# Kernel optimization log

Measured on AMD Instinct MI355X. Metric: run time of the kernel, lower is better.

Reference implementation:

```python
import jax, jax.numpy as jnp
import numpy as np

N_NODES = 50000
N_EDGES = 625000
F_IN = 128
HID = 128
N_GRAPHS = 128
N_CLASSES = 10


def _init_linear(key, fan_in, fan_out, bias=True):
    k1, k2 = jax.random.split(key)
    lim = 1.0 / np.sqrt(fan_in)
    W = jax.random.uniform(k1, (fan_in, fan_out), jnp.float32, -lim, lim)
    if bias:
        b = jax.random.uniform(k2, (fan_out,), jnp.float32, -lim, lim)
        return W, b
    return W


def setup_inputs() -> dict:
    key = jax.random.key(0)
    ks = jax.random.split(key, 12)
    x = jax.random.normal(ks[0], (N_NODES, F_IN), jnp.float32)
    edge_index = jax.random.randint(ks[1], (2, N_EDGES), 0, N_NODES, jnp.int64)
    batch = jnp.sort(jax.random.randint(ks[2], (N_NODES,), 0, N_GRAPHS, jnp.int64))
    # GraphConv k: lin_rel (weight+bias) applied to aggregated neighbors, lin_root (no bias) applied to x
    W1r, b1 = _init_linear(ks[3], F_IN, HID)
    W1s = _init_linear(ks[4], F_IN, HID, bias=False)
    W2r, b2 = _init_linear(ks[5], HID, HID)
    W2s = _init_linear(ks[6], HID, HID, bias=False)
    W3r, b3 = _init_linear(ks[7], HID, HID)
    W3s = _init_linear(ks[8], HID, HID, bias=False)
    L1w, L1b = _init_linear(ks[9], 2 * HID, 128)
    L2w, L2b = _init_linear(ks[10], 128, 64)
    L3w, L3b = _init_linear(ks[11], 64, N_CLASSES)
    return {"x": x, "edge_index": edge_index, "batch": batch,
            "W1r": W1r, "b1": b1, "W1s": W1s,
            "W2r": W2r, "b2": b2, "W2s": W2s,
            "W3r": W3r, "b3": b3, "W3s": W3s,
            "L1w": L1w, "L1b": L1b, "L2w": L2w, "L2b": L2b,
            "L3w": L3w, "L3b": L3b}


def _graph_conv(x, src, dst, Wr, br, Ws):
    # sum-aggregate source node features at destination nodes, then transform
    agg = jax.ops.segment_sum(x[src], dst, num_segments=N_NODES)  # [N, F]
    return agg @ Wr + br + x @ Ws


def _pool(x, batch):
    # cat([global_max_pool, global_mean_pool])
    mx = jax.ops.segment_max(x, batch, num_segments=N_GRAPHS)
    mx = jnp.where(jnp.isfinite(mx), mx, 0.0)  # guard empty segments
    sm = jax.ops.segment_sum(x, batch, num_segments=N_GRAPHS)
    cnt = jax.ops.segment_sum(jnp.ones((x.shape[0],), x.dtype), batch,
                              num_segments=N_GRAPHS)
    mean = sm / jnp.maximum(cnt, 1.0)[:, None]
    return jnp.concatenate([mx, mean], axis=1)  # [G, 2F]


def reference(x, edge_index, batch, W1r, b1, W1s, W2r, b2, W2s, W3r, b3, W3s,
              L1w, L1b, L2w, L2b, L3w, L3b):
    src, dst = edge_index[0], edge_index[1]
    h = jax.nn.relu(_graph_conv(x, src, dst, W1r, b1, W1s))
    x1 = _pool(h, batch)
    h = jax.nn.relu(_graph_conv(h, src, dst, W2r, b2, W2s))
    x2 = _pool(h, batch)
    h = jax.nn.relu(_graph_conv(h, src, dst, W3r, b3, W3s))
    x3 = _pool(h, batch)
    g = x1 + x2 + x3                      # [G, 256]
    g = jax.nn.relu(g @ L1w + L1b)        # dropout is identity at inference
    g = jax.nn.relu(g @ L2w + L2b)
    return jax.nn.log_softmax(g @ L3w + L3b, axis=-1)
```

## Files before the change

kernel.cpp:

```cpp
#include <hip/hip_runtime.h>
#include <math.h>

constexpr int N  = 50000;
constexpr int NE = 625000;
constexpr int F  = 128;
constexpr int NG = 128;
constexpr int NC = 10;
constexpr int CAP = 48;

typedef __attribute__((ext_vector_type(4))) float f32x4;
typedef __attribute__((ext_vector_type(8))) short bf16x8;

__device__ __forceinline__ ushort f2bf(float f) {
    unsigned u = __float_as_uint(f);
    u = (u + 0x7FFF + ((u >> 16) & 1)) >> 16;
    return (ushort)u;
}
__device__ __forceinline__ float bf_lo(unsigned u) {
    return __uint_as_float(u << 16);
}
__device__ __forceinline__ float bf_hi(unsigned u) {
    return __uint_as_float(u & 0xffff0000u);
}


__global__ __launch_bounds__(256) void k_setup(
    const float* __restrict__ x, ushort* __restrict__ xb,
    const float* __restrict__ W0, const float* __restrict__ W1,
    const float* __restrict__ W2, const float* __restrict__ W3,
    const float* __restrict__ W4, const float* __restrict__ W5,
    ushort* __restrict__ O,
    const int* __restrict__ batch, int* __restrict__ gstart,
    int* __restrict__ cnt, float* __restrict__ gpool,
    int* __restrict__ csrb, ushort* __restrict__ hA, ushort* __restrict__ hB)
{
    int b = blockIdx.x, t = threadIdx.x;
    if (b < 3125) {
        int i = (b * 256 + t) * 8;
        float4 a = *(const float4*)(x + i);
        float4 c = *(const float4*)(x + i + 4);
        ushort r[8] = {f2bf(a.x), f2bf(a.y), f2bf(a.z), f2bf(a.w),
                       f2bf(c.x), f2bf(c.y), f2bf(c.z), f2bf(c.w)};
        *(uint4*)(xb + i) = *(uint4*)r;
    } else if (b < 3509) {
        int bb = b - 3125;
        int wsel = bb >> 6;
        int i = (bb & 63) * 256 + t;
        int k = i >> 7, n = i & 127;
        const float* W = wsel == 0 ? W0 : wsel == 1 ? W1 : wsel == 2 ? W2
                       : wsel == 3 ? W3 : wsel == 4 ? W4 : W5;
        O[wsel * 16384 + n * 128 + k] = f2bf(W[k * 128 + n]);
    } else if (b == 3509) {
        int g = t;
        if (g > NG) return;
        if (g == NG) { gstart[NG] = N; return; }
        int lo = 0, hi = N;
        while (lo < hi) {
            int mid = (lo + hi) >> 1;
            if (batch[mid] < g) lo = mid + 1; else hi = mid;
        }
        gstart[g] = lo;
    } else if (b < 3706) {
        int i = (b - 3510) * 256 + t;
        if (i < N) cnt[i] = 0;
    } else if (b < 3770) {
        int i = (b - 3706) * 256 + t;
        *(uint4*)((unsigned*)gpool + i * 4) = (uint4){0, 0, 0, 0};
    } else if (b < 6114) {
        int i = (b - 3770) * 256 + t;
        if (i < N * CAP / 4)
            *(int4*)(csrb + i * 4) = (int4){N, N, N, N};
    } else {
        if (t < 48) {
            int which = t >> 4, j = t & 15;
            ushort* tab = which == 0 ? xb : which == 1 ? hA : hB;
            *(uint4*)(tab + (size_t)N * F + j * 8) = (uint4){0, 0, 0, 0};
        }
    }
}


__global__ void k_fill(const int* __restrict__ src, const int* __restrict__ dst,
                       int* __restrict__ cnt, int* __restrict__ csrb, int ne) {
    int e = blockIdx.x * blockDim.x + threadIdx.x;
    if (e < ne) {
        int d = dst[e];
        int pos = atomicAdd(&cnt[d], 1);
        if (pos < CAP) csrb[d * CAP + pos] = src[e];
    }
}


#define LDSTR 136

__global__ __launch_bounds__(256) void k_layer(
    const ushort* __restrict__ hin,
    const int* __restrict__ cnt, const int* __restrict__ csrb,
    const int* __restrict__ batch, const int* __restrict__ gstart,
    const ushort* __restrict__ WrT, const ushort* __restrict__ WsT,
    const float* __restrict__ br,
    ushort* __restrict__ hout,
    float* __restrict__ gmaxL,
    float* __restrict__ gsum,
    int nrows)
{
    __shared__ ushort sA[16][LDSTR];
    __shared__ int sbatch[16];

    const int tid = threadIdx.x;
    const int r0 = blockIdx.x * 16;
    const int wv = tid >> 6, lane = tid & 63;
    const int lo16 = lane & 15, hi = lane >> 4;

    if (tid < 16) {
        int r = r0 + tid;
        sbatch[tid] = (r < nrows) ? batch[r] : -1;
    }

    {
        int row = wv * 4 + hi;
        int v = r0 + row;
        float acc[8] = {0.f, 0.f, 0.f, 0.f, 0.f, 0.f, 0.f, 0.f};
        if (v < nrows) {
            int deg = cnt[v];
            if (deg > CAP) deg = CAP;
            const int* bucket = csrb + v * CAP;
            for (int e = 0; e < deg; e += 16) {
                int4 i0 = *(const int4*)(bucket + e);
                int4 i1 = *(const int4*)(bucket + e + 4);
                int4 i2 = *(const int4*)(bucket + e + 8);
                int4 i3 = *(const int4*)(bucket + e + 12);
                int idx[16] = {i0.x, i0.y, i0.z, i0.w, i1.x, i1.y, i1.z, i1.w,
                               i2.x, i2.y, i2.z, i2.w, i3.x, i3.y, i3.z, i3.w};
                uint4 w[16];
#pragma unroll
                for (int j = 0; j < 16; ++j)
                    w[j] = *(const uint4*)(hin + (size_t)idx[j] * F + lo16 * 8);
#pragma unroll
                for (int j = 0; j < 16; ++j) {
                    acc[0] += bf_lo(w[j].x); acc[1] += bf_hi(w[j].x);
                    acc[2] += bf_lo(w[j].y); acc[3] += bf_hi(w[j].y);
                    acc[4] += bf_lo(w[j].z); acc[5] += bf_hi(w[j].z);
                    acc[6] += bf_lo(w[j].w); acc[7] += bf_hi(w[j].w);
                }
            }
        }
        ushort r8[8];
#pragma unroll
        for (int j = 0; j < 8; ++j) r8[j] = f2bf(acc[j]);
        *(uint4*)(&sA[row][lo16 * 8]) = *(uint4*)r8;
    }

    bf16x8 af1[4];
    {
        int row = r0 + lo16;
#pragma unroll
        for (int ks = 0; ks < 4; ++ks) {
            if (row < nrows)
                af1[ks] = *(const bf16x8*)(hin + (size_t)row * F + ks * 32 + hi * 8);
            else
                af1[ks] = (bf16x8){0, 0, 0, 0, 0, 0, 0, 0};
        }
    }

    f32x4 acc2[2];
#pragma unroll
    for (int n = 0; n < 2; ++n) {
        float b = br[wv * 32 + n * 16 + lo16];
        acc2[n] = (f32x4){b, b, b, b};
    }

    __syncthreads();

#pragma unroll
    for (int ks = 0; ks < 4; ++ks) {
        int k0 = ks * 32 + hi * 8;
        bf16x8 a0 = *(const bf16x8*)(&sA[lo16][k0]);
#pragma unroll
        for (int n = 0; n < 2; ++n) {
            bf16x8 b = *(const bf16x8*)(WrT + (size_t)(wv * 32 + n * 16 + lo16) * F + k0);
            acc2[n] = __builtin_amdgcn_mfma_f32_16x16x32_bf16(a0, b, acc2[n], 0, 0, 0);
        }
    }

#pragma unroll
    for (int ks = 0; ks < 4; ++ks) {
        int k0 = ks * 32 + hi * 8;
#pragma unroll
        for (int n = 0; n < 2; ++n) {
            bf16x8 b = *(const bf16x8*)(WsT + (size_t)(wv * 32 + n * 16 + lo16) * F + k0);
            acc2[n] = __builtin_amdgcn_mfma_f32_16x16x32_bf16(af1[ks], b, acc2[n], 0, 0, 0);
        }
    }

    __syncthreads();

#pragma unroll
    for (int n = 0; n < 2; ++n) {
        int col = wv * 32 + n * 16 + lo16;
#pragma unroll
        for (int q = 0; q < 4; ++q) {
            int lrow = hi * 4 + q;
            sA[lrow][col] = f2bf(fmaxf(acc2[n][q], 0.f));
        }
    }
    __syncthreads();

    if (hout) {
        int row = tid >> 4;
        int c = (tid & 15) * 8;
        int grow = r0 + row;
        if (grow < nrows)
            *(uint4*)(hout + (size_t)grow * F + c) = *(const uint4*)(&sA[row][c]);
    }

    {
        int f = tid & 127, seg = tid >> 7;
        int curg = -1;
        float mx = 0.f, sm = 0.f;
        for (int r = seg * 8; r < seg * 8 + 8; ++r) {
            int bg = sbatch[r];
            if (bg != curg) {
                if (curg >= 0) {
                    float inv = 1.0f / (float)(gstart[curg + 1] - gstart[curg]);
                    atomicMax((int*)&gmaxL[curg * 128 + f], __float_as_int(mx));
                    atomicAdd(&gsum[curg * 128 + f], sm * inv);
                }
                curg = bg; mx = 0.f; sm = 0.f;
            }
            if (bg >= 0) {
                float v = bf_lo((unsigned)sA[r][f]);
                mx = fmaxf(mx, v);
                sm += v;
            }
        }
        if (curg >= 0) {
            float inv = 1.0f / (float)(gstart[curg + 1] - gstart[curg]);
            atomicMax((int*)&gmaxL[curg * 128 + f], __float_as_int(mx));
            atomicAdd(&gsum[curg * 128 + f], sm * inv);
        }
    }
}


__global__ __launch_bounds__(256) void k_mlp(const float* __restrict__ gpool,
                                             const float* __restrict__ L1w, const float* __restrict__ L1b,
                                             const float* __restrict__ L2w, const float* __restrict__ L2b,
                                             const float* __restrict__ L3w, const float* __restrict__ L3b,
                                             float* __restrict__ out) {
    __shared__ float gv[256], o1[128], o2[64], o3[16];
    int g = blockIdx.x, t = threadIdx.x;
    if (t < 128) {
        gv[t] = gpool[16384 + g * 128 + t] + gpool[2 * 16384 + g * 128 + t]
              + gpool[3 * 16384 + g * 128 + t];
    } else {
        gv[t] = gpool[g * 128 + (t - 128)];
    }
    __syncthreads();
    if (t < 128) {
        float a = L1b[t];
        for (int k = 0; k < 256; ++k) a += gv[k] * L1w[k * 128 + t];
        o1[t] = fmaxf(a, 0.f);
    }
    __syncthreads();
    if (t < 64) {
        float a = L2b[t];
        for (int k = 0; k < 128; ++k) a += o1[k] * L2w[k * 64 + t];
        o2[t] = fmaxf(a, 0.f);
    }
    __syncthreads();
    if (t < NC) {
        float a = L3b[t];
        for (int k = 0; k < 64; ++k) a += o2[k] * L3w[k * NC + t];
        o3[t] = a;
    }
    __syncthreads();
    if (t < NC) {
        float m = o3[0];
        for (int i = 1; i < NC; ++i) m = fmaxf(m, o3[i]);
        float s = 0.f;
        for (int i = 0; i < NC; ++i) s += expf(o3[i] - m);
        out[g * NC + t] = o3[t] - m - logf(s);
    }
}


extern "C" void kernel_launch(void* const* d_in, const int* in_sizes, int n_in,
                              void* d_out, int out_size, void* d_ws, size_t ws_size,
                              hipStream_t stream) {
    const float* x     = (const float*)d_in[0];
    const int*   ei    = (const int*)d_in[1];
    const int*   batch = (const int*)d_in[2];
    const float* W1r = (const float*)d_in[3];
    const float* b1  = (const float*)d_in[4];
    const float* W1s = (const float*)d_in[5];
    const float* W2r = (const float*)d_in[6];
    const float* b2  = (const float*)d_in[7];
    const float* W2s = (const float*)d_in[8];
    const float* W3r = (const float*)d_in[9];
    const float* b3  = (const float*)d_in[10];
    const float* W3s = (const float*)d_in[11];
    const float* L1w = (const float*)d_in[12];
    const float* L1b = (const float*)d_in[13];
    const float* L2w = (const float*)d_in[14];
    const float* L2b = (const float*)d_in[15];
    const float* L3w = (const float*)d_in[16];
    const float* L3b = (const float*)d_in[17];
    float* out = (float*)d_out;

    char* ws = (char*)d_ws;
    const size_t SZ_HB = (size_t)(N + 8) * F * sizeof(ushort);
    ushort* x_bf  = (ushort*)(ws);
    ushort* hA    = (ushort*)(ws + SZ_HB);
    ushort* hB    = (ushort*)(ws + 2 * SZ_HB);
    size_t off    = 3 * SZ_HB;
    ushort* Wt0   = (ushort*)(ws + off); off += 6 * 128 * 128 * 2;
    int* cnt      = (int*)(ws + off); off += 200704;
    int* csrb     = (int*)(ws + off); off += (size_t)N * CAP * 4;
    int* gstart   = (int*)(ws + off); off += 1024;
    float* gpool  = (float*)(ws + off); off += 4 * 16384 * 4;

    const int* src = ei;
    const int* dst = ei + NE;

    k_setup<<<6115, 256, 0, stream>>>(x, x_bf, W1r, W1s, W2r, W2s, W3r, W3s, Wt0,
                                      batch, gstart, cnt, gpool, csrb, hA, hB);

    k_fill<<<(NE + 255) / 256, 256, 0, stream>>>(src, dst, cnt, csrb, NE);

    const int NLB = (N + 15) / 16;
    ushort* Wt[6];
    for (int i = 0; i < 6; ++i) Wt[i] = Wt0 + i * 16384;

    k_layer<<<NLB, 256, 0, stream>>>(x_bf, cnt, csrb, batch, gstart,
                                     Wt[0], Wt[1], b1, hA,
                                     gpool + 16384, gpool, N);
    k_layer<<<NLB, 256, 0, stream>>>(hA, cnt, csrb, batch, gstart,
                                     Wt[2], Wt[3], b2, hB,
                                     gpool + 2 * 16384, gpool, N);
    k_layer<<<NLB, 256, 0, stream>>>(hB, cnt, csrb, batch, gstart,
                                     Wt[4], Wt[5], b3, (ushort*)nullptr,
                                     gpool + 3 * 16384, gpool, N);

    k_mlp<<<NG, 256, 0, stream>>>(gpool, L1w, L1b, L2w, L2b, L3w, L3b, out);
}
```

Measured before the change: 204.6 us.

## Split layer into column-blocked gather and conv-pool kernels with 16-bit edge indices

Node feature tables are stored column-blocked (four 32-feature slabs of 64 bytes per node), so each gather pass touches a smaller slab that fits cache better. Neighbor aggregation moves into a separate k_gather kernel that reduces across lanes with shuffles and writes an aggregate buffer. A k_convpool kernel then runs the MFMA transform and pooling. Bucket indices shrink to ushort, which relies on N fitting in 16 bits. The cost is an extra aggregate write and read per layer plus three more kernel launches.

```diff
diff --git a/kernel.cpp b/kernel.cpp
--- a/kernel.cpp
+++ b/kernel.cpp
@@ -1,26 +1,35 @@
 #include <hip/hip_runtime.h>
 #include <math.h>
 
-constexpr int N  = 50000;
-constexpr int NE = 625000;
-constexpr int F  = 128;
-constexpr int NG = 128;
-constexpr int NC = 10;
+constexpr int N   = 50000;
+constexpr int NP1 = N + 1;
+constexpr int NE  = 625000;
+constexpr int F   = 128;
+constexpr int NG  = 128;
+constexpr int NC  = 10;
 constexpr int CAP = 48;
 
 typedef __attribute__((ext_vector_type(4))) float f32x4;
 typedef __attribute__((ext_vector_type(8))) short bf16x8;
+typedef __attribute__((ext_vector_type(4))) unsigned u32x4;
 
 __device__ __forceinline__ ushort f2bf(float f) {
     unsigned u = __float_as_uint(f);
     u = (u + 0x7FFF + ((u >> 16) & 1)) >> 16;
     return (ushort)u;
 }
-__device__ __forceinline__ float bf_lo(unsigned u) {
-    return __uint_as_float(u << 16);
-}
-__device__ __forceinline__ float bf_hi(unsigned u) {
-    return __uint_as_float(u & 0xffff0000u);
+__device__ __forceinline__ float bf_lo(unsigned u) { return __uint_as_float(u << 16); }
+__device__ __forceinline__ float bf_hi(unsigned u) { return __uint_as_float(u & 0xffff0000u); }
+
+__device__ __forceinline__ size_t tIdx(int cb, int node, int off) {
+    return ((size_t)cb * NP1 + node) * 32 + off;
+}
+
+__device__ __forceinline__ void accum8(float* acc, uint4 w) {
+    acc[0] += bf_lo(w.x); acc[1] += bf_hi(w.x);
+    acc[2] += bf_lo(w.y); acc[3] += bf_hi(w.y);
+    acc[4] += bf_lo(w.z); acc[5] += bf_hi(w.z);
+    acc[6] += bf_lo(w.w); acc[7] += bf_hi(w.w);
 }
 
 
@@ -32,16 +41,19 @@
     ushort* __restrict__ O,
     const int* __restrict__ batch, int* __restrict__ gstart,
     int* __restrict__ cnt, float* __restrict__ gpool,
-    int* __restrict__ csrb, ushort* __restrict__ hA, ushort* __restrict__ hB)
+    ushort* __restrict__ bkt, ushort* __restrict__ hA, ushort* __restrict__ hB)
 {
     int b = blockIdx.x, t = threadIdx.x;
     if (b < 3125) {
-        int i = (b * 256 + t) * 8;
-        float4 a = *(const float4*)(x + i);
-        float4 c = *(const float4*)(x + i + 4);
+        int i = b * 256 + t;
+        int node = i >> 4, col8 = i & 15;
+        int c0 = col8 * 8;
+        const float* xp = x + (size_t)node * F + c0;
+        float4 a = *(const float4*)(xp);
+        float4 c = *(const float4*)(xp + 4);
         ushort r[8] = {f2bf(a.x), f2bf(a.y), f2bf(a.z), f2bf(a.w),
                        f2bf(c.x), f2bf(c.y), f2bf(c.z), f2bf(c.w)};
-        *(uint4*)(xb + i) = *(uint4*)r;
+        *(uint4*)(xb + tIdx(c0 >> 5, node, c0 & 31)) = *(uint4*)r;
     } else if (b < 3509) {
         int bb = b - 3125;
         int wsel = bb >> 6;
@@ -66,43 +78,93 @@
     } else if (b < 3770) {
         int i = (b - 3706) * 256 + t;
         *(uint4*)((unsigned*)gpool + i * 4) = (uint4){0, 0, 0, 0};
-    } else if (b < 6114) {
+    } else if (b < 4942) {
         int i = (b - 3770) * 256 + t;
-        if (i < N * CAP / 4)
-            *(int4*)(csrb + i * 4) = (int4){N, N, N, N};
+        if (i < N * CAP / 8) {
+            unsigned p = 0xC350C350u;
+            *(uint4*)(bkt + (size_t)i * 8) = (uint4){p, p, p, p};
+        }
     } else {
         if (t < 48) {
-            int which = t >> 4, j = t & 15;
-            ushort* tab = which == 0 ? xb : which == 1 ? hA : hB;
-            *(uint4*)(tab + (size_t)N * F + j * 8) = (uint4){0, 0, 0, 0};
+            int table = t >> 4, r = t & 15;
+            int cb = r >> 2, j = r & 3;
+            ushort* tab = table == 0 ? xb : table == 1 ? hA : hB;
+            *(uint4*)(tab + tIdx(cb, N, j * 8)) = (uint4){0, 0, 0, 0};
         }
     }
 }
 
 
 __global__ void k_fill(const int* __restrict__ src, const int* __restrict__ dst,
-                       int* __restrict__ cnt, int* __restrict__ csrb, int ne) {
+                       int* __restrict__ cnt, ushort* __restrict__ bkt, int ne) {
     int e = blockIdx.x * blockDim.x + threadIdx.x;
     if (e < ne) {
         int d = dst[e];
         int pos = atomicAdd(&cnt[d], 1);
-        if (pos < CAP) csrb[d * CAP + pos] = src[e];
+        if (pos < CAP) bkt[(size_t)d * CAP + pos] = (ushort)src[e];
+    }
+}
+
+
+__global__ __launch_bounds__(256) void k_gather(
+    const ushort* __restrict__ tab, const int* __restrict__ cnt,
+    const ushort* __restrict__ bkt, ushort* __restrict__ aggB)
+{
+    const int b = blockIdx.x;
+    const int cb = b / 6250;
+    const int nb = b - cb * 6250;
+    const int tid = threadIdx.x;
+    const int lane = tid & 63, wv = tid >> 6;
+    const int g  = lane >> 5;
+    const int e8 = (lane >> 2) & 7;
+    const int j  = lane & 3;
+
+    const int v = nb * 8 + wv * 2 + g;
+    const int deg = min(cnt[v], CAP);
+    const ushort* bucket = bkt + (size_t)v * CAP;
+    const ushort* tcb = tab + (size_t)cb * NP1 * 32;
+
+    float acc[8] = {0.f, 0.f, 0.f, 0.f, 0.f, 0.f, 0.f, 0.f};
+
+    int i0 = __builtin_nontemporal_load(bucket + e8);
+    int i1 = __builtin_nontemporal_load(bucket + 8 + e8);
+    uint4 w0 = *(const uint4*)(tcb + (size_t)i0 * 32 + j * 8);
+    uint4 w1 = *(const uint4*)(tcb + (size_t)i1 * 32 + j * 8);
+    accum8(acc, w0);
+    accum8(acc, w1);
+
+    for (int e = 16; e < deg; e += 8) {
+        int ii = __builtin_nontemporal_load(bucket + e + e8);
+        uint4 w = *(const uint4*)(tcb + (size_t)ii * 32 + j * 8);
+        accum8(acc, w);
+    }
+
+#pragma unroll
+    for (int k = 0; k < 8; ++k) {
+        acc[k] += __shfl_xor(acc[k], 4, 64);
+        acc[k] += __shfl_xor(acc[k], 8, 64);
+        acc[k] += __shfl_xor(acc[k], 16, 64);
+    }
+
+    if ((lane & 28) == 0) {
+        ushort r8[8];
+#pragma unroll
+        for (int k = 0; k < 8; ++k) r8[k] = f2bf(acc[k]);
+        u32x4 val = *(u32x4*)r8;
+        __builtin_nontemporal_store(val, (u32x4*)(aggB + tIdx(cb, v, j * 8)));
     }
 }
 
 
 #define LDSTR 136
 
-__global__ __launch_bounds__(256) void k_layer(
-    const ushort* __restrict__ hin,
-    const int* __restrict__ cnt, const int* __restrict__ csrb,
+__global__ __launch_bounds__(256) void k_convpool(
+    const ushort* __restrict__ aggB, const ushort* __restrict__ hinB,
     const int* __restrict__ batch, const int* __restrict__ gstart,
     const ushort* __restrict__ WrT, const ushort* __restrict__ WsT,
     const float* __restrict__ br,
-    ushort* __restrict__ hout,
-    float* __restrict__ gmaxL,
-    float* __restrict__ gsum,
-    int nrows)
+    ushort* __restrict__ houtB,
+    float* __restrict__ gmaxL, float* __restrict__ gsum)
 {
     __shared__ ushort sA[16][LDSTR];
     __shared__ int sbatch[16];
@@ -112,55 +174,14 @@
     const int wv = tid >> 6, lane = tid & 63;
     const int lo16 = lane & 15, hi = lane >> 4;
 
-    if (tid < 16) {
-        int r = r0 + tid;
-        sbatch[tid] = (r < nrows) ? batch[r] : -1;
-    }
-
-    {
-        int row = wv * 4 + hi;
-        int v = r0 + row;
-        float acc[8] = {0.f, 0.f, 0.f, 0.f, 0.f, 0.f, 0.f, 0.f};
-        if (v < nrows) {
-            int deg = cnt[v];
-            if (deg > CAP) deg = CAP;
-            const int* bucket = csrb + v * CAP;
-            for (int e = 0; e < deg; e += 16) {
-                int4 i0 = *(const int4*)(bucket + e);
-                int4 i1 = *(const int4*)(bucket + e + 4);
-                int4 i2 = *(const int4*)(bucket + e + 8);
-                int4 i3 = *(const int4*)(bucket + e + 12);
-                int idx[16] = {i0.x, i0.y, i0.z, i0.w, i1.x, i1.y, i1.z, i1.w,
-                               i2.x, i2.y, i2.z, i2.w, i3.x, i3.y, i3.z, i3.w};
-                uint4 w[16];
-#pragma unroll
-                for (int j = 0; j < 16; ++j)
-                    w[j] = *(const uint4*)(hin + (size_t)idx[j] * F + lo16 * 8);
-#pragma unroll
-                for (int j = 0; j < 16; ++j) {
-                    acc[0] += bf_lo(w[j].x); acc[1] += bf_hi(w[j].x);
-                    acc[2] += bf_lo(w[j].y); acc[3] += bf_hi(w[j].y);
-                    acc[4] += bf_lo(w[j].z); acc[5] += bf_hi(w[j].z);
-                    acc[6] += bf_lo(w[j].w); acc[7] += bf_hi(w[j].w);
-                }
-            }
-        }
-        ushort r8[8];
-#pragma unroll
-        for (int j = 0; j < 8; ++j) r8[j] = f2bf(acc[j]);
-        *(uint4*)(&sA[row][lo16 * 8]) = *(uint4*)r8;
-    }
-
-    bf16x8 af1[4];
-    {
-        int row = r0 + lo16;
-#pragma unroll
-        for (int ks = 0; ks < 4; ++ks) {
-            if (row < nrows)
-                af1[ks] = *(const bf16x8*)(hin + (size_t)row * F + ks * 32 + hi * 8);
-            else
-                af1[ks] = (bf16x8){0, 0, 0, 0, 0, 0, 0, 0};
-        }
+    if (tid < 16) sbatch[tid] = batch[r0 + tid];
+
+    const int rowa = r0 + lo16;
+    bf16x8 af0[4], af1[4];
+#pragma unroll
+    for (int ks = 0; ks < 4; ++ks) {
+        af0[ks] = *(const bf16x8*)(aggB + tIdx(ks, rowa, hi * 8));
+        af1[ks] = *(const bf16x8*)(hinB + tIdx(ks, rowa, hi * 8));
     }
 
     f32x4 acc2[2];
@@ -170,49 +191,39 @@
         acc2[n] = (f32x4){b, b, b, b};
     }
 
-    __syncthreads();
-
 #pragma unroll
     for (int ks = 0; ks < 4; ++ks) {
         int k0 = ks * 32 + hi * 8;
-        bf16x8 a0 = *(const bf16x8*)(&sA[lo16][k0]);
 #pragma unroll
         for (int n = 0; n < 2; ++n) {
-            bf16x8 b = *(const bf16x8*)(WrT + (size_t)(wv * 32 + n * 16 + lo16) * F + k0);
-            acc2[n] = __builtin_amdgcn_mfma_f32_16x16x32_bf16(a0, b, acc2[n], 0, 0, 0);
-        }
-    }
-
+            bf16x8 bR = *(const bf16x8*)(WrT + (size_t)(wv * 32 + n * 16 + lo16) * F + k0);
+            acc2[n] = __builtin_amdgcn_mfma_f32_16x16x32_bf16(af0[ks], bR, acc2[n], 0, 0, 0);
+        }
+    }
 #pragma unroll
     for (int ks = 0; ks < 4; ++ks) {
         int k0 = ks * 32 + hi * 8;
 #pragma unroll
         for (int n = 0; n < 2; ++n) {
-            bf16x8 b = *(const bf16x8*)(WsT + (size_t)(wv * 32 + n * 16 + lo16) * F + k0);
-            acc2[n] = __builtin_amdgcn_mfma_f32_16x16x32_bf16(af1[ks], b, acc2[n], 0, 0, 0);
-        }
-    }
-
-    __syncthreads();
+            bf16x8 bS = *(const bf16x8*)(WsT + (size_t)(wv * 32 + n * 16 + lo16) * F + k0);
+            acc2[n] = __builtin_amdgcn_mfma_f32_16x16x32_bf16(af1[ks], bS, acc2[n], 0, 0, 0);
+        }
+    }
 
 #pragma unroll
     for (int n = 0; n < 2; ++n) {
         int col = wv * 32 + n * 16 + lo16;
 #pragma unroll
-        for (int q = 0; q < 4; ++q) {
-            int lrow = hi * 4 + q;
-            sA[lrow][col] = f2bf(fmaxf(acc2[n][q], 0.f));
-        }
-    }
-    __syncthreads();
-
-    if (hout) {
-        int row = tid >> 4;
-        int c = (tid & 15) * 8;
-        int grow = r0 + row;
-        if (grow < nrows)
-            *(uint4*)(hout + (size_t)grow * F + c) = *(const uint4*)(&sA[row][c]);
-    }
+        for (int q = 0; q < 4; ++q)
+            sA[hi * 4 + q][col] = f2bf(fmaxf(acc2[n][q], 0.f));
+    }
+
+    if (houtB) {
+        int ns = lane >> 2, jj = lane & 3;
+        uint4 val = *(const uint4*)(&sA[ns][wv * 32 + jj * 8]);
+        *(uint4*)(houtB + tIdx(wv, r0 + ns, jj * 8)) = val;
+    }
+    __syncthreads();
 
     {
         int f = tid & 127, seg = tid >> 7;
@@ -228,11 +239,9 @@
                 }
                 curg = bg; mx = 0.f; sm = 0.f;
             }
-            if (bg >= 0) {
-                float v = bf_lo((unsigned)sA[r][f]);
-                mx = fmaxf(mx, v);
-                sm += v;
-            }
+            float v = bf_lo((unsigned)sA[r][f]);
+            mx = fmaxf(mx, v);
+            sm += v;
         }
         if (curg >= 0) {
             float inv = 1.0f / (float)(gstart[curg + 1] - gstart[curg]);
@@ -309,38 +318,39 @@
     float* out = (float*)d_out;
 
     char* ws = (char*)d_ws;
-    const size_t SZ_HB = (size_t)(N + 8) * F * sizeof(ushort);
+    const size_t SZ_TAB = (size_t)4 * NP1 * 32 * sizeof(ushort);
     ushort* x_bf  = (ushort*)(ws);
-    ushort* hA    = (ushort*)(ws + SZ_HB);
-    ushort* hB    = (ushort*)(ws + 2 * SZ_HB);
-    size_t off    = 3 * SZ_HB;
+    ushort* hA    = (ushort*)(ws + SZ_TAB);
+    ushort* hB    = (ushort*)(ws + 2 * SZ_TAB);
+    ushort* agg   = (ushort*)(ws + 3 * SZ_TAB);
+    size_t off    = 4 * SZ_TAB;
     ushort* Wt0   = (ushort*)(ws + off); off += 6 * 128 * 128 * 2;
     int* cnt      = (int*)(ws + off); off += 200704;
-    int* csrb     = (int*)(ws + off); off += (size_t)N * CAP * 4;
+    ushort* bkt   = (ushort*)(ws + off); off += (size_t)N * CAP * 2 + 256;
     int* gstart   = (int*)(ws + off); off += 1024;
     float* gpool  = (float*)(ws + off); off += 4 * 16384 * 4;
 
     const int* src = ei;
     const int* dst = ei + NE;
 
-    k_setup<<<6115, 256, 0, stream>>>(x, x_bf, W1r, W1s, W2r, W2s, W3r, W3s, Wt0,
-                                      batch, gstart, cnt, gpool, csrb, hA, hB);
-
-    k_fill<<<(NE + 255) / 256, 256, 0, stream>>>(src, dst, cnt, csrb, NE);
-
-    const int NLB = (N + 15) / 16;
+    k_setup<<<4943, 256, 0, stream>>>(x, x_bf, W1r, W1s, W2r, W2s, W3r, W3s, Wt0,
+                                      batch, gstart, cnt, gpool, bkt, hA, hB);
+    k_fill<<<(NE + 255) / 256, 256, 0, stream>>>(src, dst, cnt, bkt, NE);
+
     ushort* Wt[6];
     for (int i = 0; i < 6; ++i) Wt[i] = Wt0 + i * 16384;
-
-    k_layer<<<NLB, 256, 0, stream>>>(x_bf, cnt, csrb, batch, gstart,
-                                     Wt[0], Wt[1], b1, hA,
-                                     gpool + 16384, gpool, N);
-    k_layer<<<NLB, 256, 0, stream>>>(hA, cnt, csrb, batch, gstart,
-                                     Wt[2], Wt[3], b2, hB,
-                                     gpool + 2 * 16384, gpool, N);
-    k_layer<<<NLB, 256, 0, stream>>>(hB, cnt, csrb, batch, gstart,
-                                     Wt[4], Wt[5], b3, (ushort*)nullptr,
-                                     gpool + 3 * 16384, gpool, N);
+    const int NGB = 4 * 6250;
+    const int NCB = N / 16;
+
+    k_gather<<<NGB, 256, 0, stream>>>(x_bf, cnt, bkt, agg);
+    k_convpool<<<NCB, 256, 0, stream>>>(agg, x_bf, batch, gstart, Wt[0], Wt[1], b1,
+                                        hA, gpool + 16384, gpool);
+    k_gather<<<NGB, 256, 0, stream>>>(hA, cnt, bkt, agg);
+    k_convpool<<<NCB, 256, 0, stream>>>(agg, hA, batch, gstart, Wt[2], Wt[3], b2,
+                                        hB, gpool + 2 * 16384, gpool);
+    k_gather<<<NGB, 256, 0, stream>>>(hB, cnt, bkt, agg);
+    k_convpool<<<NCB, 256, 0, stream>>>(agg, hB, batch, gstart, Wt[4], Wt[5], b3,
+                                        (ushort*)nullptr, gpool + 3 * 16384, gpool);
 
     k_mlp<<<NG, 256, 0, stream>>>(gpool, L1w, L1b, L2w, L2b, L3w, L3b, out);
 }
```

New measurement: 264.1 us. +29.1%, slower.

## Store neighbor buckets as 16-bit indices and fuse edge fill into prep kernel

Applied to the files above, without the earlier changes.

Neighbor bucket indices are stored as 16-bit values instead of 32-bit, halving bucket memory for init, fill and the three layer gathers. The edge bucket fill is merged into the setup kernel, and a small separate init kernel now does the count and bucket clearing. Node indices up to 50000 fit in 16 bits, with 50000 (0xC350) used as the padding sentinel. This adds an extra launch and ties the code to a node count below 65536.

```diff
diff --git a/kernel.cpp b/kernel.cpp
--- a/kernel.cpp
+++ b/kernel.cpp
@@ -1,11 +1,11 @@
 #include <hip/hip_runtime.h>
 #include <math.h>
 
-constexpr int N  = 50000;
-constexpr int NE = 625000;
-constexpr int F  = 128;
-constexpr int NG = 128;
-constexpr int NC = 10;
+constexpr int N   = 50000;
+constexpr int NE  = 625000;
+constexpr int F   = 128;
+constexpr int NG  = 128;
+constexpr int NC  = 10;
 constexpr int CAP = 48;
 
 typedef __attribute__((ext_vector_type(4))) float f32x4;
@@ -16,41 +16,67 @@
     u = (u + 0x7FFF + ((u >> 16) & 1)) >> 16;
     return (ushort)u;
 }
-__device__ __forceinline__ float bf_lo(unsigned u) {
-    return __uint_as_float(u << 16);
-}
-__device__ __forceinline__ float bf_hi(unsigned u) {
-    return __uint_as_float(u & 0xffff0000u);
-}
-
-
-__global__ __launch_bounds__(256) void k_setup(
+__device__ __forceinline__ float bf_lo(unsigned u) { return __uint_as_float(u << 16); }
+__device__ __forceinline__ float bf_hi(unsigned u) { return __uint_as_float(u & 0xffff0000u); }
+
+__device__ __forceinline__ void accum8(float* acc, uint4 w) {
+    acc[0] += bf_lo(w.x); acc[1] += bf_hi(w.x);
+    acc[2] += bf_lo(w.y); acc[3] += bf_hi(w.y);
+    acc[4] += bf_lo(w.z); acc[5] += bf_hi(w.z);
+    acc[6] += bf_lo(w.w); acc[7] += bf_hi(w.w);
+}
+
+
+__global__ __launch_bounds__(256) void k_init(int* __restrict__ cnt,
+                                              ushort* __restrict__ bkt) {
+    int i = blockIdx.x * 256 + threadIdx.x;
+    const int NBKT = N * CAP / 8;
+    if (i < NBKT) {
+        unsigned p = 0xC350C350u;
+        *(uint4*)(bkt + (size_t)i * 8) = (uint4){p, p, p, p};
+    } else if (i < NBKT + 12512) {
+        int c = i - NBKT;
+        if (c * 4 < N + 4) *(uint4*)((unsigned*)cnt + c * 4) = (uint4){0, 0, 0, 0};
+    }
+}
+
+
+__global__ __launch_bounds__(256) void k_prep(
+    const int* __restrict__ src, const int* __restrict__ dst,
+    int* __restrict__ cnt, ushort* __restrict__ bkt,
     const float* __restrict__ x, ushort* __restrict__ xb,
     const float* __restrict__ W0, const float* __restrict__ W1,
     const float* __restrict__ W2, const float* __restrict__ W3,
     const float* __restrict__ W4, const float* __restrict__ W5,
     ushort* __restrict__ O,
     const int* __restrict__ batch, int* __restrict__ gstart,
-    int* __restrict__ cnt, float* __restrict__ gpool,
-    int* __restrict__ csrb, ushort* __restrict__ hA, ushort* __restrict__ hB)
+    float* __restrict__ gpool,
+    ushort* __restrict__ hA, ushort* __restrict__ hB)
 {
     int b = blockIdx.x, t = threadIdx.x;
-    if (b < 3125) {
-        int i = (b * 256 + t) * 8;
+    if (b < 2442) {
+        int e = b * 256 + t;
+        if (e < NE) {
+            int d = dst[e];
+            int pos = atomicAdd(&cnt[d], 1);
+            if (pos < CAP) bkt[(size_t)d * CAP + pos] = (ushort)src[e];
+        }
+    } else if (b < 5567) {
+        int i = ((b - 2442) * 256 + t) * 8;
         float4 a = *(const float4*)(x + i);
         float4 c = *(const float4*)(x + i + 4);
         ushort r[8] = {f2bf(a.x), f2bf(a.y), f2bf(a.z), f2bf(a.w),
                        f2bf(c.x), f2bf(c.y), f2bf(c.z), f2bf(c.w)};
         *(uint4*)(xb + i) = *(uint4*)r;
-    } else if (b < 3509) {
-        int bb = b - 3125;
+    } else if (b < 5951) {
+        int bb = b - 5567;
         int wsel = bb >> 6;
         int i = (bb & 63) * 256 + t;
         int k = i >> 7, n = i & 127;
         const float* W = wsel == 0 ? W0 : wsel == 1 ? W1 : wsel == 2 ? W2
                        : wsel == 3 ? W3 : wsel == 4 ? W4 : W5;
         O[wsel * 16384 + n * 128 + k] = f2bf(W[k * 128 + n]);
-    } else if (b == 3509) {
+    } else if (b == 5951) {
         int g = t;
         if (g > NG) return;
         if (g == NG) { gstart[NG] = N; return; }
@@ -60,33 +86,15 @@
             if (batch[mid] < g) lo = mid + 1; else hi = mid;
         }
         gstart[g] = lo;
-    } else if (b < 3706) {
-        int i = (b - 3510) * 256 + t;
-        if (i < N) cnt[i] = 0;
-    } else if (b < 3770) {
-        int i = (b - 3706) * 256 + t;
+    } else if (b < 6016) {
+        int i = (b - 5952) * 256 + t;
         *(uint4*)((unsigned*)gpool + i * 4) = (uint4){0, 0, 0, 0};
-    } else if (b < 6114) {
-        int i = (b - 3770) * 256 + t;
-        if (i < N * CAP / 4)
-            *(int4*)(csrb + i * 4) = (int4){N, N, N, N};
     } else {
         if (t < 48) {
-            int which = t >> 4, j = t & 15;
-            ushort* tab = which == 0 ? xb : which == 1 ? hA : hB;
+            int table = t >> 4, j = t & 15;
+            ushort* tab = table == 0 ? xb : table == 1 ? hA : hB;
             *(uint4*)(tab + (size_t)N * F + j * 8) = (uint4){0, 0, 0, 0};
         }
-    }
-}
-
-
-__global__ void k_fill(const int* __restrict__ src, const int* __restrict__ dst,
-                       int* __restrict__ cnt, int* __restrict__ csrb, int ne) {
-    int e = blockIdx.x * blockDim.x + threadIdx.x;
-    if (e < ne) {
-        int d = dst[e];
-        int pos = atomicAdd(&cnt[d], 1);
-        if (pos < CAP) csrb[d * CAP + pos] = src[e];
     }
 }
 
@@ -95,7 +103,7 @@
 
 __global__ __launch_bounds__(256) void k_layer(
     const ushort* __restrict__ hin,
-    const int* __restrict__ cnt, const int* __restrict__ csrb,
+    const int* __restrict__ cnt, const ushort* __restrict__ bkt,
     const int* __restrict__ batch, const int* __restrict__ gstart,
     const ushort* __restrict__ WrT, const ushort* __restrict__ WsT,
     const float* __restrict__ br,
@@ -122,27 +130,24 @@
         int v = r0 + row;
         float acc[8] = {0.f, 0.f, 0.f, 0.f, 0.f, 0.f, 0.f, 0.f};
         if (v < nrows) {
-            int deg = cnt[v];
-            if (deg > CAP) deg = CAP;
-            const int* bucket = csrb + v * CAP;
+            int deg = min(cnt[v], CAP);
+            const ushort* bucket = bkt + (size_t)v * CAP;
             for (int e = 0; e < deg; e += 16) {
-                int4 i0 = *(const int4*)(bucket + e);
-                int4 i1 = *(const int4*)(bucket + e + 4);
-                int4 i2 = *(const int4*)(bucket + e + 8);
-                int4 i3 = *(const int4*)(bucket + e + 12);
-                int idx[16] = {i0.x, i0.y, i0.z, i0.w, i1.x, i1.y, i1.z, i1.w,
-                               i2.x, i2.y, i2.z, i2.w, i3.x, i3.y, i3.z, i3.w};
+                uint4 p0 = *(const uint4*)(bucket + e);
+                uint4 p1 = *(const uint4*)(bucket + e + 8);
+                unsigned dw[8] = {p0.x, p0.y, p0.z, p0.w, p1.x, p1.y, p1.z, p1.w};
+                int idx[16];
+#pragma unroll
+                for (int j = 0; j < 8; ++j) {
+                    idx[2 * j]     = dw[j] & 0xffffu;
+                    idx[2 * j + 1] = dw[j] >> 16;
+                }
                 uint4 w[16];
 #pragma unroll
                 for (int j = 0; j < 16; ++j)
                     w[j] = *(const uint4*)(hin + (size_t)idx[j] * F + lo16 * 8);
 #pragma unroll
-                for (int j = 0; j < 16; ++j) {
-                    acc[0] += bf_lo(w[j].x); acc[1] += bf_hi(w[j].x);
-                    acc[2] += bf_lo(w[j].y); acc[3] += bf_hi(w[j].y);
-                    acc[4] += bf_lo(w[j].z); acc[5] += bf_hi(w[j].z);
-                    acc[6] += bf_lo(w[j].w); acc[7] += bf_hi(w[j].w);
-                }
+                for (int j = 0; j < 16; ++j) accum8(acc, w[j]);
             }
         }
         ushort r8[8];
@@ -316,29 +321,29 @@
     size_t off    = 3 * SZ_HB;
     ushort* Wt0   = (ushort*)(ws + off); off += 6 * 128 * 128 * 2;
     int* cnt      = (int*)(ws + off); off += 200704;
-    int* csrb     = (int*)(ws + off); off += (size_t)N * CAP * 4;
+    ushort* bkt   = (ushort*)(ws + off); off += (size_t)N * CAP * 2 + 256;
     int* gstart   = (int*)(ws + off); off += 1024;
     float* gpool  = (float*)(ws + off); off += 4 * 16384 * 4;
 
     const int* src = ei;
     const int* dst = ei + NE;
 
-    k_setup<<<6115, 256, 0, stream>>>(x, x_bf, W1r, W1s, W2r, W2s, W3r, W3s, Wt0,
-                                      batch, gstart, cnt, gpool, csrb, hA, hB);
-
-    k_fill<<<(NE + 255) / 256, 256, 0, stream>>>(src, dst, cnt, csrb, NE);
-
-    const int NLB = (N + 15) / 16;
+    k_init<<<1222, 256, 0, stream>>>(cnt, bkt);
+    k_prep<<<6017, 256, 0, stream>>>(src, dst, cnt, bkt, x, x_bf,
+                                     W1r, W1s, W2r, W2s, W3r, W3s, Wt0,
+                                     batch, gstart, gpool, hA, hB);
+
     ushort* Wt[6];
     for (int i = 0; i < 6; ++i) Wt[i] = Wt0 + i * 16384;
-
-    k_layer<<<NLB, 256, 0, stream>>>(x_bf, cnt, csrb, batch, gstart,
+    const int NLB = (N + 15) / 16;
+
+    k_layer<<<NLB, 256, 0, stream>>>(x_bf, cnt, bkt, batch, gstart,
                                      Wt[0], Wt[1], b1, hA,
                                      gpool + 16384, gpool, N);
-    k_layer<<<NLB, 256, 0, stream>>>(hA, cnt, csrb, batch, gstart,
+    k_layer<<<NLB, 256, 0, stream>>>(hA, cnt, bkt, batch, gstart,
                                      Wt[2], Wt[3], b2, hB,
                                      gpool + 2 * 16384, gpool, N);
-    k_layer<<<NLB, 256, 0, stream>>>(hB, cnt, csrb, batch, gstart,
+    k_layer<<<NLB, 256, 0, stream>>>(hB, cnt, bkt, batch, gstart,
                                      Wt[4], Wt[5], b3, (ushort*)nullptr,
                                      gpool + 3 * 16384, gpool, N);
 
```

Result: no change. 204.4 us (-0.1%).
